# Kernel optimization log

Measured on AMD Instinct MI355X. Metric: run time of the kernel, lower is better.

Reference implementation:

```python
import jax, jax.numpy as jnp
import numpy as np

N = 2048       # num nodes
IN = 512       # in_features == hidden_features == out_features (residuals)
HID = 512
OUT = 512
H = 8          # num_heads
DX = 256       # x feature dim
LN_EPS = 1e-5
NORM_EPS = 1e-12


def _layernorm(x, g, b):
    mu = jnp.mean(x, axis=-1, keepdims=True)
    var = jnp.mean(jnp.square(x - mu), axis=-1, keepdims=True)
    return (x - mu) * jax.lax.rsqrt(var + LN_EPS) * g + b


def _l1_normalize(x):
    # torch F.normalize(p=1): x / max(||x||_1, eps)
    n = jnp.sum(jnp.abs(x), axis=-1, keepdims=True)
    return x / jnp.maximum(n, NORM_EPS)


def _linear_init(key, out_f, in_f):
    kw, kb = jax.random.split(key)
    bound = 1.0 / np.sqrt(in_f)
    W = jax.random.uniform(kw, (out_f, in_f), jnp.float32, -bound, bound)
    b = jax.random.uniform(kb, (out_f,), jnp.float32, -bound, bound)
    return W, b


def setup_inputs() -> dict:
    key = jax.random.key(0)
    ks = jax.random.split(key, 10)
    h = jax.random.normal(ks[0], (N, IN), jnp.float32)
    x = jax.random.uniform(ks[1], (N, DX), jnp.float32)
    Wk, bk = _linear_init(ks[2], HID, IN)
    Wq, bq = _linear_init(ks[3], HID, IN)
    Wv, bv = _linear_init(ks[4], HID, IN)
    Wm1, bm1 = _linear_init(ks[5], H, H + 1)   # mixing_x2h
    Wm2, bm2 = _linear_init(ks[6], 1, H)
    Wfc, bfc = _linear_init(ks[7], OUT, HID + 4)
    ln_g = jnp.ones((IN,), jnp.float32)
    ln_b = jnp.zeros((IN,), jnp.float32)
    lnf_g = jnp.ones((HID,), jnp.float32)
    lnf_b = jnp.zeros((HID,), jnp.float32)
    return dict(h=h, x=x, ln_g=ln_g, ln_b=ln_b, Wk=Wk, bk=bk, Wq=Wq, bq=bq,
                Wv=Wv, bv=bv, Wm1=Wm1, bm1=bm1, Wm2=Wm2, bm2=bm2,
                lnf_g=lnf_g, lnf_b=lnf_b, Wfc=Wfc, bfc=bfc)


def reference(h, x, ln_g, ln_b, Wk, bk, Wq, bq, Wv, bv, Wm1, bm1, Wm2, bm2,
              lnf_g, lnf_b, Wfc, bfc):
    h0, x0 = h, x
    hn = _layernorm(h, ln_g, ln_b)
    xn = _l1_normalize(x)

    k = (hn @ Wk.T + bk).reshape(N, HID // H, H)
    q = (hn @ Wq.T + bq).reshape(N, HID // H, H)
    a_h = jnp.einsum('xyb,zyb->xzb', k, q)          # [N, N, H]
    a_x = xn @ xn.T                                  # [N, N]

    # head mixing: Linear(H+1 -> H) over concat([a_x, a_h])
    a_cat = jnp.concatenate([a_x[..., None], a_h], axis=-1)  # [N, N, H+1]
    a_h = a_cat @ Wm1.T + bm1                                # [N, N, H]
    a_x = (a_h @ Wm2.T + bm2)[..., 0] + a_x                  # [N, N]

    a_h = jax.nn.softmax(a_h, axis=-1)               # softmax over heads
    a_x = _l1_normalize(a_x)

    # per-row stats of a_x -> [N, 4]
    i = jnp.concatenate([
        jnp.diagonal(a_x)[:, None],
        jnp.sum(a_x, axis=-1, keepdims=True),
        jnp.std(a_x, axis=-1, ddof=1, keepdims=True),
        jnp.max(a_x, axis=-1, keepdims=True),
    ], axis=-1)

    v = (hn @ Wv.T + bv).reshape(N, OUT // H, H)
    hm = jnp.einsum('xyb,yzb->xzb', a_h, v).reshape(N, HID)
    xm = a_x @ xn

    hm = hm + h0
    xm = xm + x0
    _h0 = hm

    hf = _layernorm(hm, lnf_g, lnf_b)
    hf = jnp.concatenate([hf, i], axis=-1)           # [N, HID+4]
    hf = jax.nn.elu(hf @ Wfc.T + bfc)
    hf = hf + _h0
    return (hf, xm)
```

## Files before the change

### kernel.cpp

```cpp
#include <hip/hip_runtime.h>
#include <math.h>

#define NN 2048
#define FD 512
#define DXF 256
#define JC 8
#define CHKJ (NN/JC)
#define ITI 32
#define JTW 64
#define NIT (CHKJ/JTW)
#define KC (NN/4)

typedef unsigned short u16;
typedef unsigned int u32;
typedef __attribute__((ext_vector_type(8))) short s16x8;
typedef __attribute__((ext_vector_type(4))) float f32x4;

__device__ __forceinline__ f32x4 MFMA16(s16x8 a, s16x8 b, f32x4 c) {
  return __builtin_amdgcn_mfma_f32_16x16x32_bf16(a, b, c, 0, 0, 0);
}
__device__ __forceinline__ float blo(u32 u) { return __uint_as_float(u << 16); }
__device__ __forceinline__ float bhi(u32 u) { return __uint_as_float(u & 0xffff0000u); }
__device__ __forceinline__ float b2f(u16 v) { return __uint_as_float((u32)v << 16); }
__device__ __forceinline__ u16 bf1(float f) {
  u32 u = __float_as_uint(f);
  u += 0x7fffu + ((u >> 16) & 1u);
  return (u16)(u >> 16);
}
__device__ __forceinline__ u32 pkbf(float a, float b) {
  u32 ua = __float_as_uint(a), ub = __float_as_uint(b);
  ua += 0x7fffu + ((ua >> 16) & 1u);
  ub += 0x7fffu + ((ub >> 16) & 1u);
  return (ua >> 16) | (ub & 0xffff0000u);
}

__global__ void preproc_k(
    const float* __restrict__ h, const float* __restrict__ ln_g,
    const float* __restrict__ ln_b, u16* __restrict__ hnB,
    const float* __restrict__ x, u16* __restrict__ xnB,
    const float* __restrict__ Wk, const float* __restrict__ Wq,
    const float* __restrict__ Wv, u16* __restrict__ wkB, u16* __restrict__ wqB,
    u16* __restrict__ wvB, const float* __restrict__ Wfc, u16* __restrict__ wfcB) {
  int bid = blockIdx.x, t = threadIdx.x;
  __shared__ float red[4][2];
  if (bid < NN) {
    int r = bid;
    float2 v = ((const float2*)(h + (size_t)r * FD))[t];
    float2 w = make_float2(v.x + v.y, v.x * v.x + v.y * v.y);
#pragma unroll
    for (int o = 32; o > 0; o >>= 1) { w.x += __shfl_xor(w.x, o); w.y += __shfl_xor(w.y, o); }
    if ((t & 63) == 0) { red[t >> 6][0] = w.x; red[t >> 6][1] = w.y; }
    __syncthreads();
    float S  = (red[0][0] + red[1][0]) + (red[2][0] + red[3][0]);
    float SQ = (red[0][1] + red[1][1]) + (red[2][1] + red[3][1]);
    float mean = S * (1.f / FD);
    float var  = SQ * (1.f / FD) - mean * mean;
    float rs = rsqrtf(var + 1e-5f);
    float2 gg = ((const float2*)ln_g)[t], bb = ((const float2*)ln_b)[t];
    float ox = (v.x - mean) * rs * gg.x + bb.x;
    float oy = (v.y - mean) * rs * gg.y + bb.y;
    *(u32*)(hnB + (size_t)r * FD + 2 * t) = pkbf(ox, oy);
  } else if (bid < 2 * NN) {
    int r = bid - NN;
    float v = x[(size_t)r * DXF + t];
    float s = fabsf(v);
#pragma unroll
    for (int o = 32; o > 0; o >>= 1) s += __shfl_xor(s, o);
    if ((t & 63) == 0) red[t >> 6][0] = s;
    __syncthreads();
    float S = (red[0][0] + red[1][0]) + (red[2][0] + red[3][0]);
    float inv = 1.f / fmaxf(S, 1e-12f);
    xnB[(size_t)r * DXF + t] = bf1(v * inv);
  } else if (bid < 2 * NN + 1536) {
    int idx = bid - 2 * NN;
    int z = idx >> 9;
    int i = ((idx & 511) << 8) + t;
    const float* W = (z == 0) ? Wk : (z == 1) ? Wq : Wv;
    u16* O = (z == 0) ? wkB : (z == 1) ? wqB : wvB;
    float2 v = ((const float2*)W)[i];
    ((u32*)O)[i] = pkbf(v.x, v.y);
  } else {
    int i = (bid - (2 * NN + 1536)) * 256 + t;
    if (i < 512 * 272) {
      int r = i / 272, c2 = (i - r * 272) * 2;
      float a = (c2 < 516) ? Wfc[r * 516 + c2] : 0.f;
      float b = (c2 + 1 < 516) ? Wfc[r * 516 + c2 + 1] : 0.f;
      ((u32*)wfcB)[i] = pkbf(a, b);
    }
  }
}

__global__ void xnt_k(const u16* __restrict__ xnB, u16* __restrict__ xnTg) {
  __shared__ u16 tile[16][264];
  int t = threadIdx.x;
  int r0 = blockIdx.x * 16;
#pragma unroll
  for (int s = 0; s < 2; ++s) {
    int c = s * 256 + t;
    int db = c & 31, row = c >> 5;
    *(uint4*)&tile[row][db * 8] = *(const uint4*)(xnB + (size_t)(r0 + row) * DXF + db * 8);
  }
  __syncthreads();
#pragma unroll
  for (int s = 0; s < 2; ++s) {
    int c = s * 256 + t;
    int jb = c & 1, d = c >> 1;
    u32 p[4];
#pragma unroll
    for (int e2 = 0; e2 < 4; ++e2) {
      u16 a = tile[jb * 8 + e2 * 2][d], b = tile[jb * 8 + e2 * 2 + 1][d];
      p[e2] = (u32)a | ((u32)b << 16);
    }
    *(uint4*)(xnTg + (size_t)d * NN + r0 + jb * 8) = make_uint4(p[0], p[1], p[2], p[3]);
  }
}

__global__ __launch_bounds__(256) void proj3_k(
    const u16* __restrict__ A,
    const u16* __restrict__ W0, const u16* __restrict__ W1, const u16* __restrict__ W2,
    const float* __restrict__ b0, const float* __restrict__ b1, const float* __restrict__ b2,
    u16* __restrict__ kP, u16* __restrict__ qP, u16* __restrict__ vPT) {
  int z = blockIdx.z;
  const u16* B = (z == 0) ? W0 : (z == 1) ? W1 : W2;
  const float* bias = (z == 0) ? b0 : (z == 1) ? b1 : b2;
  int t = threadIdx.x, w = t >> 6, lane = t & 63, g = lane >> 4, li = lane & 15;
  int m0 = blockIdx.x * 64 + (w & 1) * 32;
  int n0 = blockIdx.y * 64 + (w >> 1) * 32;
  f32x4 acc[2][2] = {};
  for (int k0 = 0; k0 < FD; k0 += 32) {
    s16x8 a0 = *(const s16x8*)(A + (size_t)(m0 + li) * FD + k0 + g * 8);
    s16x8 a1 = *(const s16x8*)(A + (size_t)(m0 + 16 + li) * FD + k0 + g * 8);
    s16x8 bA = *(const s16x8*)(B + (size_t)(n0 + li) * FD + k0 + g * 8);
    s16x8 bB = *(const s16x8*)(B + (size_t)(n0 + 16 + li) * FD + k0 + g * 8);
    acc[0][0] = MFMA16(a0, bA, acc[0][0]);
    acc[0][1] = MFMA16(a0, bB, acc[0][1]);
    acc[1][0] = MFMA16(a1, bA, acc[1][0]);
    acc[1][1] = MFMA16(a1, bB, acc[1][1]);
  }
#pragma unroll
  for (int ms = 0; ms < 2; ++ms)
#pragma unroll
    for (int ns = 0; ns < 2; ++ns) {
      int ncol = n0 + ns * 16 + li;
      float bv = bias[ncol];
      if (z < 2) {
        u16* out = z ? qP : kP;
#pragma unroll
        for (int r = 0; r < 4; ++r) {
          int i = m0 + ms * 16 + g * 4 + r;
          out[((size_t)(ncol & 7) * NN + i) * 64 + (ncol >> 3)] = bf1(acc[ms][ns][r] + bv);
        }
      } else {
        u16 e[4];
#pragma unroll
        for (int r = 0; r < 4; ++r) e[r] = bf1(acc[ms][ns][r] + bv);
        u32 p0 = (u32)e[0] | ((u32)e[1] << 16);
        u32 p1 = (u32)e[2] | ((u32)e[3] << 16);
        int ib = m0 + ms * 16 + g * 4;
        *(uint2*)(vPT + ((size_t)((ncol & 7) * 64 + (ncol >> 3))) * NN + ib) =
            make_uint2(p0, p1);
      }
    }
}

__global__ __launch_bounds__(256) void fc_gemm_k(
    const u16* __restrict__ A, const u16* __restrict__ B,
    const float* __restrict__ bias, const float* __restrict__ res,
    float* __restrict__ C) {
  int t = threadIdx.x, w = t >> 6, lane = t & 63, g = lane >> 4, li = lane & 15;
  int m0 = blockIdx.x * 32 + (w & 1) * 16;
  int n0 = blockIdx.y * 32 + (w >> 1) * 16;
  f32x4 acc = {};
  for (int k0 = 0; k0 < 544; k0 += 32) {
    s16x8 a0 = *(const s16x8*)(A + (size_t)(m0 + li) * 544 + k0 + g * 8);
    s16x8 b0 = *(const s16x8*)(B + (size_t)(n0 + li) * 544 + k0 + g * 8);
    acc = MFMA16(a0, b0, acc);
  }
  int ncol = n0 + li;
  float bv = bias[ncol];
#pragma unroll
  for (int r = 0; r < 4; ++r) {
    int i = m0 + g * 4 + r;
    float cv = acc[r] + bv;
    cv = (cv > 0.f) ? cv : (expf(cv) - 1.f);
    cv += res[(size_t)i * FD + ncol];
    C[(size_t)i * FD + ncol] = cv;
  }
}

__global__ __launch_bounds__(256) void xm_split_k(
    const u16* __restrict__ axg, const u16* __restrict__ xnTg,
    float* __restrict__ xmp, float* __restrict__ stq) {
  int t = threadIdx.x, w = t >> 6, lane = t & 63, g = lane >> 4, li = lane & 15;
  int m0 = blockIdx.x * 64 + (w & 1) * 32;
  int n0 = blockIdx.y * 64 + (w >> 1) * 32;
  int z = blockIdx.z;
  const int kb = z * KC;
  f32x4 acc[2][2] = {};
  float sab[2] = {0.f, 0.f}, ssu[2] = {0.f, 0.f}, ssq[2] = {0.f, 0.f};
  float smx[2] = {-1e30f, -1e30f};
  const bool do_stats = (blockIdx.y == 0) && ((w >> 1) == 0);
  for (int k0 = 0; k0 < KC; k0 += 32) {
    s16x8 a0 = *(const s16x8*)(axg + (size_t)(m0 + li) * NN + kb + k0 + g * 8);
    s16x8 a1 = *(const s16x8*)(axg + (size_t)(m0 + 16 + li) * NN + kb + k0 + g * 8);
    s16x8 bA = *(const s16x8*)(xnTg + (size_t)(n0 + li) * NN + kb + k0 + g * 8);
    s16x8 bB = *(const s16x8*)(xnTg + (size_t)(n0 + 16 + li) * NN + kb + k0 + g * 8);
    acc[0][0] = MFMA16(a0, bA, acc[0][0]);
    acc[0][1] = MFMA16(a0, bB, acc[0][1]);
    acc[1][0] = MFMA16(a1, bA, acc[1][0]);
    acc[1][1] = MFMA16(a1, bB, acc[1][1]);
    if (do_stats) {
#pragma unroll
      for (int ms = 0; ms < 2; ++ms) {
        u32 pu[4];
        *(s16x8*)pu = ms ? a1 : a0;
#pragma unroll
        for (int q2 = 0; q2 < 4; ++q2) {
          float x0 = blo(pu[q2]), x1 = bhi(pu[q2]);
          sab[ms] += fabsf(x0) + fabsf(x1);
          ssu[ms] += x0 + x1;
          ssq[ms] += x0 * x0 + x1 * x1;
          smx[ms] = fmaxf(smx[ms], fmaxf(x0, x1));
        }
      }
    }
  }
  if (do_stats) {
#pragma unroll
    for (int off = 16; off < 64; off <<= 1) {
#pragma unroll
      for (int ms = 0; ms < 2; ++ms) {
        sab[ms] += __shfl_xor(sab[ms], off);
        ssu[ms] += __shfl_xor(ssu[ms], off);
        ssq[ms] += __shfl_xor(ssq[ms], off);
        smx[ms] = fmaxf(smx[ms], __shfl_xor(smx[ms], off));
      }
    }
    if (g == 0) {
#pragma unroll
      for (int ms = 0; ms < 2; ++ms) {
        size_t base = ((size_t)z * NN + m0 + ms * 16 + li) * 4;
        stq[base + 0] = sab[ms]; stq[base + 1] = ssu[ms];
        stq[base + 2] = ssq[ms]; stq[base + 3] = smx[ms];
      }
    }
  }
#pragma unroll
  for (int ms = 0; ms < 2; ++ms)
#pragma unroll
    for (int ns = 0; ns < 2; ++ns) {
      int ncol = n0 + ns * 16 + li;
#pragma unroll
      for (int r = 0; r < 4; ++r) {
        int i = m0 + ms * 16 + g * 4 + r;
        xmp[(size_t)z * NN * DXF + (size_t)i * DXF + ncol] = acc[ms][ns][r];
      }
    }
}

__global__ __launch_bounds__(512, 2) void fused_mfma_k(
    const u16* __restrict__ kP, const u16* __restrict__ qP,
    const u16* __restrict__ vPT, const u16* __restrict__ xnB,
    const float* __restrict__ Wm1, const float* __restrict__ bm1,
    const float* __restrict__ Wm2, const float* __restrict__ bm2,
    u16* __restrict__ hmPart, u16* __restrict__ axg, float* __restrict__ stPd) {
  __shared__ __align__(16) unsigned char L[81920];
  const int O_KI = 0, O_XNI = 32768, O_P = 49152;
  const int t = threadIdx.x, w = t >> 6, lane = t & 63;
  const int g = lane >> 4, li = lane & 15;
  const int i0 = blockIdx.x * ITI, chunk = blockIdx.y;
  const int si = w & 1;
  const int jL = (w >> 1) * 16 + li;
  const int iRow = si * 16 + li;

  float W1[8][9], B1v[8], w2v[8];
#pragma unroll
  for (int o = 0; o < 8; ++o) {
    B1v[o] = bm1[o];
    w2v[o] = Wm2[o];
#pragma unroll
    for (int b3 = 0; b3 < 9; ++b3) W1[o][b3] = Wm1[o * 9 + b3];
  }
  const float b2v = bm2[0];

#pragma unroll
  for (int s = 0; s < 4; ++s) {
    int c = s * 512 + t;
    int yb = c & 7, il = (c >> 3) & 31, b = c >> 8;
    uint4 v = *(const uint4*)(kP + ((size_t)b * NN + i0 + il) * 64 + yb * 8);
    *(uint4*)(L + O_KI + b * 4096 + il * 128 + ((yb ^ (il & 7)) << 4)) = v;
  }
#pragma unroll
  for (int s = 0; s < 2; ++s) {
    int c = s * 512 + t;
    int db = c & 31, il = c >> 5;
    uint4 v = *(const uint4*)(xnB + (size_t)(i0 + il) * DXF + db * 8);
    *(uint4*)(L + O_XNI + il * 512 + ((db ^ (il & 7)) << 4)) = v;
  }
  __syncthreads();

  f32x4 hmA[2][4];
#pragma unroll
  for (int a = 0; a < 2; ++a)
#pragma unroll
    for (int c = 0; c < 4; ++c) hmA[a][c] = (f32x4)(0.f);

  for (int it = 0; it < NIT; ++it) {
    const int j0 = chunk * CHKJ + it * JTW;
    f32x4 accS[9];
#pragma unroll
    for (int a = 0; a < 9; ++a) accS[a] = (f32x4)(0.f);
#pragma unroll
    for (int b = 0; b < 8; ++b)
#pragma unroll
      for (int ks = 0; ks < 2; ++ks) {
        int blk = ks * 4 + g;
        s16x8 af = *(const s16x8*)(L + O_KI + b * 4096 + iRow * 128 +
                                   ((blk ^ (iRow & 7)) << 4));
        s16x8 bf = *(const s16x8*)(qP + ((size_t)b * NN + j0 + jL) * 64 + ks * 32 + g * 8);
        accS[b] = MFMA16(af, bf, accS[b]);
      }
#pragma unroll
    for (int ks = 0; ks < 8; ++ks) {
      int blk = ks * 4 + g;
      s16x8 af = *(const s16x8*)(L + O_XNI + iRow * 512 + ((blk ^ (iRow & 7)) << 4));
      s16x8 bf = *(const s16x8*)(xnB + (size_t)(j0 + jL) * DXF + ks * 32 + g * 8);
      accS[8] = MFMA16(af, bf, accS[8]);
    }
    __syncthreads();
#pragma unroll
    for (int r = 0; r < 4; ++r) {
      float sb[8];
#pragma unroll
      for (int b = 0; b < 8; ++b) sb[b] = accS[b][r];
      float ax = accS[8][r];
      float m[8];
#pragma unroll
      for (int o = 0; o < 8; ++o) {
        float a = B1v[o] + W1[o][0] * ax;
#pragma unroll
        for (int b = 0; b < 8; ++b) a += W1[o][1 + b] * sb[b];
        m[o] = a;
      }
      float axn = b2v + ax;
#pragma unroll
      for (int o = 0; o < 8; ++o) axn += w2v[o] * m[o];
      const int iL2 = si * 16 + g * 4 + r;
      const int iG = i0 + iL2, jG = j0 + jL;
      axg[(size_t)iG * NN + jG] = bf1(axn);
      if (iG == jG) stPd[iG] = axn;
      float mx = m[0];
#pragma unroll
      for (int o = 1; o < 8; ++o) mx = fmaxf(mx, m[o]);
      float es[8], esum = 0.f;
#pragma unroll
      for (int o = 0; o < 8; ++o) { es[o] = __expf(m[o] - mx); esum += es[o]; }
      float inv = 1.f / esum;
      const int base = iL2 * 128 + (((jL >> 3) ^ (iL2 & 7)) << 4) + (jL & 7) * 2;
#pragma unroll
      for (int b = 0; b < 8; ++b)
        *(u16*)(L + O_P + b * 4096 + base) = bf1(es[b] * inv);
    }
    __syncthreads();
#pragma unroll
    for (int hh = 0; hh < 2; ++hh) {
      const int hd = (w >> 1) * 2 + hh;
#pragma unroll
      for (int kb = 0; kb < 2; ++kb) {
        const int prow = si * 16 + li;
        s16x8 pa = *(const s16x8*)(L + O_P + hd * 4096 + prow * 128 +
                                   (((kb * 4 + g) ^ (prow & 7)) << 4));
#pragma unroll
        for (int zt = 0; zt < 4; ++zt) {
          s16x8 vf = *(const s16x8*)(vPT + ((size_t)hd * 64 + zt * 16 + li) * NN +
                                     j0 + kb * 32 + g * 8);
          hmA[hh][zt] = MFMA16(pa, vf, hmA[hh][zt]);
        }
      }
    }
  }
#pragma unroll
  for (int hh = 0; hh < 2; ++hh) {
    const int hd = (w >> 1) * 2 + hh;
#pragma unroll
    for (int zt = 0; zt < 4; ++zt)
#pragma unroll
      for (int r = 0; r < 4; ++r) {
        int i = i0 + si * 16 + g * 4 + r;
        int z = zt * 16 + li;
        hmPart[((size_t)(chunk * 8 + hd) * NN + i) * 64 + z] = bf1(hmA[hh][zt][r]);
      }
  }
}

__global__ void epilogue1_k(
    const float* __restrict__ h, const float* __restrict__ x,
    const u16* __restrict__ hmp, const float* __restrict__ xmp,
    const float* __restrict__ stq, const float* __restrict__ stPd,
    const float* __restrict__ lnf_g, const float* __restrict__ lnf_b,
    float* __restrict__ hmf, u16* __restrict__ hfeB, float* __restrict__ out_xm) {
  int r = blockIdx.x, t = threadIdx.x;
  int c0 = 2 * t, c1 = c0 + 1;
  float2 acc = ((const float2*)(h + (size_t)r * FD))[t];
#pragma unroll
  for (int ch = 0; ch < JC; ++ch) {
    acc.x += b2f(hmp[((size_t)(ch * 8 + (c0 & 7)) * NN + r) * 64 + (c0 >> 3)]);
    acc.y += b2f(hmp[((size_t)(ch * 8 + (c1 & 7)) * NN + r) * 64 + (c1 >> 3)]);
  }
  ((float2*)(hmf + (size_t)r * FD))[t] = acc;
  float2 w = make_float2(acc.x + acc.y, acc.x * acc.x + acc.y * acc.y);
#pragma unroll
  for (int o = 32; o > 0; o >>= 1) { w.x += __shfl_xor(w.x, o); w.y += __shfl_xor(w.y, o); }
  __shared__ float red[4][2];
  __shared__ float s_inv;
  if ((t & 63) == 0) { red[t >> 6][0] = w.x; red[t >> 6][1] = w.y; }
  __syncthreads();
  float S  = (red[0][0] + red[1][0]) + (red[2][0] + red[3][0]);
  float SQ = (red[0][1] + red[1][1]) + (red[2][1] + red[3][1]);
  float mean = S * (1.f / FD);
  float var  = SQ * (1.f / FD) - mean * mean;
  float rs = rsqrtf(var + 1e-5f);
  float2 g2 = ((const float2*)lnf_g)[t], b2 = ((const float2*)lnf_b)[t];
  float ox = (acc.x - mean) * rs * g2.x + b2.x;
  float oy = (acc.y - mean) * rs * g2.y + b2.y;
  *(u32*)(hfeB + (size_t)r * 544 + c0) = pkbf(ox, oy);
  if (t == 0) {
    float sab = 0.f, ssu = 0.f, ssq = 0.f, smx = -1e30f;
#pragma unroll
    for (int c = 0; c < 4; ++c) {
      size_t b = ((size_t)c * NN + r) * 4;
      sab += stq[b + 0]; ssu += stq[b + 1]; ssq += stq[b + 2];
      smx = fmaxf(smx, stq[b + 3]);
    }
    float diag = stPd[r];
    float L1 = fmaxf(sab, 1e-12f);
    float inv = 1.f / L1;
    float stdv = sqrtf(fmaxf((ssq - ssu * ssu * (1.f / 2048.f)) * (1.f / 2047.f), 0.f)) * inv;
    u16* he = hfeB + (size_t)r * 544;
    he[512] = bf1(diag * inv); he[513] = bf1(ssu * inv);
    he[514] = bf1(stdv);       he[515] = bf1(smx * inv);
    s_inv = inv;
  }
  if (t < 14) *(u32*)(hfeB + (size_t)r * 544 + 516 + 2 * t) = 0;
  __syncthreads();
  float inv = s_inv;
  float xv = xmp[(size_t)r * DXF + t] + xmp[(size_t)NN * DXF + (size_t)r * DXF + t] +
             xmp[2 * (size_t)NN * DXF + (size_t)r * DXF + t] +
             xmp[3 * (size_t)NN * DXF + (size_t)r * DXF + t];
  out_xm[(size_t)r * DXF + t] = xv * inv + x[(size_t)r * DXF + t];
}

extern "C" void kernel_launch(void* const* d_in, const int* in_sizes, int n_in,
                              void* d_out, int out_size, void* d_ws, size_t ws_size,
                              hipStream_t stream) {
  (void)in_sizes; (void)n_in; (void)out_size; (void)ws_size;
  const float* h    = (const float*)d_in[0];
  const float* x    = (const float*)d_in[1];
  const float* ln_g = (const float*)d_in[2];
  const float* ln_b = (const float*)d_in[3];
  const float* Wk   = (const float*)d_in[4];
  const float* bk   = (const float*)d_in[5];
  const float* Wq   = (const float*)d_in[6];
  const float* bq   = (const float*)d_in[7];
  const float* Wv   = (const float*)d_in[8];
  const float* bv   = (const float*)d_in[9];
  const float* Wm1  = (const float*)d_in[10];
  const float* bm1  = (const float*)d_in[11];
  const float* Wm2  = (const float*)d_in[12];
  const float* bm2  = (const float*)d_in[13];
  const float* lnf_g = (const float*)d_in[14];
  const float* lnf_b = (const float*)d_in[15];
  const float* Wfc  = (const float*)d_in[16];
  const float* bfc  = (const float*)d_in[17];

  char* wsb = (char*)d_ws;
  size_t off = 0;
  auto alloc = [&](size_t bytes) { char* p = wsb + off; off += (bytes + 255) & ~(size_t)255; return p; };
  u16*   hnB  = (u16*)alloc((size_t)NN * FD * 2);
  u16*   wkB  = (u16*)alloc((size_t)FD * FD * 2);
  u16*   wqB  = (u16*)alloc((size_t)FD * FD * 2);
  u16*   wvB  = (u16*)alloc((size_t)FD * FD * 2);
  u16*   wfcB = (u16*)alloc((size_t)512 * 544 * 2);
  u16*   kP   = (u16*)alloc((size_t)8 * NN * 64 * 2);
  u16*   qP   = (u16*)alloc((size_t)8 * NN * 64 * 2);
  u16*   vPT  = (u16*)alloc((size_t)8 * 64 * NN * 2);
  u16*   xnB  = (u16*)alloc((size_t)NN * DXF * 2);
  u16*   xnTg = (u16*)alloc((size_t)DXF * NN * 2);
  u16*   axg  = (u16*)alloc((size_t)NN * NN * 2);
  u16*   hmp  = (u16*)alloc((size_t)JC * 8 * NN * 64 * 2);
  float* xmp  = (float*)alloc((size_t)4 * NN * DXF * 4);
  float* stq  = (float*)alloc((size_t)4 * NN * 4 * 4);
  float* stPd = (float*)alloc((size_t)NN * 4);
  float* hmf  = (float*)alloc((size_t)NN * FD * 4);
  u16*   hfeB = (u16*)alloc((size_t)NN * 544 * 2);
  float* out_hf = (float*)d_out;
  float* out_xm = out_hf + (size_t)NN * FD;

  preproc_k<<<2 * NN + 1536 + 544, 256, 0, stream>>>(
      h, ln_g, ln_b, hnB, x, xnB, Wk, Wq, Wv, wkB, wqB, wvB, Wfc, wfcB);
  xnt_k<<<NN / 16, 256, 0, stream>>>(xnB, xnTg);

  proj3_k<<<dim3(32, 8, 3), 256, 0, stream>>>(hnB, wkB, wqB, wvB, bk, bq, bv, kP, qP, vPT);

  fused_mfma_k<<<dim3(NN / ITI, JC), 512, 0, stream>>>(kP, qP, vPT, xnB, Wm1, bm1, Wm2, bm2,
                                                       axg ? hmp : hmp, axg, stPd);

  xm_split_k<<<dim3(32, 4, 4), 256, 0, stream>>>(axg, xnTg, xmp, stq);

  epilogue1_k<<<NN, 256, 0, stream>>>(h, x, hmp, xmp, stq, stPd, lnf_g, lnf_b, hmf, hfeB, out_xm);

  fc_gemm_k<<<dim3(64, 16), 256, 0, stream>>>(hfeB, wfcB, bfc, hmf, out_hf);
}
```

Baseline: 174.2 us.

## Double-buffer softmax tile in LDS, defer PV MFMA, fold head-mixing algebra

The P (softmax-over-heads) tile now lives in a double-buffered LDS region, and the P·V MFMA for the previous j-tile runs at the start of the next iteration. This removes one __syncthreads per iteration and lets the score MFMAs overlap the PV work. The K and xn row tiles are no longer staged in LDS and are read directly from global/L1 each iteration, which cuts LDS use from 80 KB to 64 KB. The a_x update is precomputed as a linear combination of the raw scores instead of being summed over the mixed heads, saving some FMAs but adding repeated global loads.

```diff
diff --git a/kernel.cpp b/kernel.cpp
--- a/kernel.cpp
+++ b/kernel.cpp
@@ -264,40 +264,38 @@
     const float* __restrict__ Wm1, const float* __restrict__ bm1,
     const float* __restrict__ Wm2, const float* __restrict__ bm2,
     u16* __restrict__ hmPart, u16* __restrict__ axg, float* __restrict__ stPd) {
-  __shared__ __align__(16) unsigned char L[81920];
-  const int O_KI = 0, O_XNI = 32768, O_P = 49152;
+  __shared__ __align__(16) unsigned char L[65536];
   const int t = threadIdx.x, w = t >> 6, lane = t & 63;
   const int g = lane >> 4, li = lane & 15;
   const int i0 = blockIdx.x * ITI, chunk = blockIdx.y;
   const int si = w & 1;
-  const int jL = (w >> 1) * 16 + li;
+  const int jw = w >> 1;
+  const int jL = jw * 16 + li;
   const int iRow = si * 16 + li;
-
-  float W1[8][9], B1v[8], w2v[8];
-#pragma unroll
-  for (int o = 0; o < 8; ++o) {
-    B1v[o] = bm1[o];
-    w2v[o] = Wm2[o];
-#pragma unroll
-    for (int b3 = 0; b3 < 9; ++b3) W1[o][b3] = Wm1[o * 9 + b3];
-  }
-  const float b2v = bm2[0];
-
-#pragma unroll
-  for (int s = 0; s < 4; ++s) {
-    int c = s * 512 + t;
-    int yb = c & 7, il = (c >> 3) & 31, b = c >> 8;
-    uint4 v = *(const uint4*)(kP + ((size_t)b * NN + i0 + il) * 64 + yb * 8);
-    *(uint4*)(L + O_KI + b * 4096 + il * 128 + ((yb ^ (il & 7)) << 4)) = v;
-  }
-#pragma unroll
-  for (int s = 0; s < 2; ++s) {
-    int c = s * 512 + t;
-    int db = c & 31, il = c >> 5;
-    uint4 v = *(const uint4*)(xnB + (size_t)(i0 + il) * DXF + db * 8);
-    *(uint4*)(L + O_XNI + il * 512 + ((db ^ (il & 7)) << 4)) = v;
-  }
-  __syncthreads();
+  const int prow = si * 16 + li;
+
+  float W1[8][9], B1v[8];
+  float C0, Cax, Cb[8];
+  {
+    float w2v[8];
+#pragma unroll
+    for (int o = 0; o < 8; ++o) {
+      B1v[o] = bm1[o];
+      w2v[o] = Wm2[o];
+#pragma unroll
+      for (int b3 = 0; b3 < 9; ++b3) W1[o][b3] = Wm1[o * 9 + b3];
+    }
+    C0 = bm2[0]; Cax = 1.f;
+#pragma unroll
+    for (int b = 0; b < 8; ++b) Cb[b] = 0.f;
+#pragma unroll
+    for (int o = 0; o < 8; ++o) {
+      C0 += w2v[o] * B1v[o];
+      Cax += w2v[o] * W1[o][0];
+#pragma unroll
+      for (int b = 0; b < 8; ++b) Cb[b] += w2v[o] * W1[o][1 + b];
+    }
+  }
 
   f32x4 hmA[2][4];
 #pragma unroll
@@ -305,8 +303,27 @@
 #pragma unroll
     for (int c = 0; c < 4; ++c) hmA[a][c] = (f32x4)(0.f);
 
+  int j0prev = 0;
   for (int it = 0; it < NIT; ++it) {
     const int j0 = chunk * CHKJ + it * JTW;
+    if (it > 0) {
+      const unsigned char* Pb = L + (((it - 1) & 1) << 15);
+#pragma unroll
+      for (int hh = 0; hh < 2; ++hh) {
+        const int hd = jw * 2 + hh;
+#pragma unroll
+        for (int kb = 0; kb < 2; ++kb) {
+          s16x8 pa = *(const s16x8*)(Pb + hd * 4096 + prow * 128 +
+                                     (((kb * 4 + g) ^ (prow & 7)) << 4));
+#pragma unroll
+          for (int zt = 0; zt < 4; ++zt) {
+            s16x8 vf = *(const s16x8*)(vPT + ((size_t)hd * 64 + zt * 16 + li) * NN +
+                                       j0prev + kb * 32 + g * 8);
+            hmA[hh][zt] = MFMA16(pa, vf, hmA[hh][zt]);
+          }
+        }
+      }
+    }
     f32x4 accS[9];
 #pragma unroll
     for (int a = 0; a < 9; ++a) accS[a] = (f32x4)(0.f);
@@ -314,26 +331,26 @@
     for (int b = 0; b < 8; ++b)
 #pragma unroll
       for (int ks = 0; ks < 2; ++ks) {
-        int blk = ks * 4 + g;
-        s16x8 af = *(const s16x8*)(L + O_KI + b * 4096 + iRow * 128 +
-                                   ((blk ^ (iRow & 7)) << 4));
+        s16x8 af = *(const s16x8*)(kP + ((size_t)b * NN + i0 + iRow) * 64 + ks * 32 + g * 8);
         s16x8 bf = *(const s16x8*)(qP + ((size_t)b * NN + j0 + jL) * 64 + ks * 32 + g * 8);
         accS[b] = MFMA16(af, bf, accS[b]);
       }
 #pragma unroll
     for (int ks = 0; ks < 8; ++ks) {
-      int blk = ks * 4 + g;
-      s16x8 af = *(const s16x8*)(L + O_XNI + iRow * 512 + ((blk ^ (iRow & 7)) << 4));
+      s16x8 af = *(const s16x8*)(xnB + (size_t)(i0 + iRow) * DXF + ks * 32 + g * 8);
       s16x8 bf = *(const s16x8*)(xnB + (size_t)(j0 + jL) * DXF + ks * 32 + g * 8);
       accS[8] = MFMA16(af, bf, accS[8]);
     }
-    __syncthreads();
+    unsigned char* Pw = L + ((it & 1) << 15);
 #pragma unroll
     for (int r = 0; r < 4; ++r) {
       float sb[8];
 #pragma unroll
       for (int b = 0; b < 8; ++b) sb[b] = accS[b][r];
       float ax = accS[8][r];
+      float axn = C0 + Cax * ax;
+#pragma unroll
+      for (int b = 0; b < 8; ++b) axn += Cb[b] * sb[b];
       float m[8];
 #pragma unroll
       for (int o = 0; o < 8; ++o) {
@@ -342,9 +359,6 @@
         for (int b = 0; b < 8; ++b) a += W1[o][1 + b] * sb[b];
         m[o] = a;
       }
-      float axn = b2v + ax;
-#pragma unroll
-      for (int o = 0; o < 8; ++o) axn += w2v[o] * m[o];
       const int iL2 = si * 16 + g * 4 + r;
       const int iG = i0 + iL2, jG = j0 + jL;
       axg[(size_t)iG * NN + jG] = bf1(axn);
@@ -359,21 +373,24 @@
       const int base = iL2 * 128 + (((jL >> 3) ^ (iL2 & 7)) << 4) + (jL & 7) * 2;
 #pragma unroll
       for (int b = 0; b < 8; ++b)
-        *(u16*)(L + O_P + b * 4096 + base) = bf1(es[b] * inv);
+        *(u16*)(Pw + b * 4096 + base) = bf1(es[b] * inv);
     }
     __syncthreads();
+    j0prev = j0;
+  }
+  {
+    const unsigned char* Pb = L + (((NIT - 1) & 1) << 15);
 #pragma unroll
     for (int hh = 0; hh < 2; ++hh) {
-      const int hd = (w >> 1) * 2 + hh;
+      const int hd = jw * 2 + hh;
 #pragma unroll
       for (int kb = 0; kb < 2; ++kb) {
-        const int prow = si * 16 + li;
-        s16x8 pa = *(const s16x8*)(L + O_P + hd * 4096 + prow * 128 +
+        s16x8 pa = *(const s16x8*)(Pb + hd * 4096 + prow * 128 +
                                    (((kb * 4 + g) ^ (prow & 7)) << 4));
 #pragma unroll
         for (int zt = 0; zt < 4; ++zt) {
           s16x8 vf = *(const s16x8*)(vPT + ((size_t)hd * 64 + zt * 16 + li) * NN +
-                                     j0 + kb * 32 + g * 8);
+                                     j0prev + kb * 32 + g * 8);
           hmA[hh][zt] = MFMA16(pa, vf, hmA[hh][zt]);
         }
       }
@@ -381,7 +398,7 @@
   }
 #pragma unroll
   for (int hh = 0; hh < 2; ++hh) {
-    const int hd = (w >> 1) * 2 + hh;
+    const int hd = jw * 2 + hh;
 #pragma unroll
     for (int zt = 0; zt < 4; ++zt)
 #pragma unroll
@@ -503,7 +520,7 @@
   proj3_k<<<dim3(32, 8, 3), 256, 0, stream>>>(hnB, wkB, wqB, wvB, bk, bq, bv, kP, qP, vPT);
 
   fused_mfma_k<<<dim3(NN / ITI, JC), 512, 0, stream>>>(kP, qP, vPT, xnB, Wm1, bm1, Wm2, bm2,
-                                                       axg ? hmp : hmp, axg, stPd);
+                                                       hmp, axg, stPd);
 
   xm_split_k<<<dim3(32, 4, 4), 256, 0, stream>>>(axg, xnTg, xmp, stq);
 
```

After: 186.3 us. 1.07x slower.
